# Kernel tuning notes

Measured on AMD Instinct MI355X. Metric: run time of the kernel, lower is better.

## Reference

```python
import jax, jax.numpy as jnp
import numpy as np

# dims: batch, seq(tokens, excl cls), input_dim, embed_dim, heads, ffn, experts, proto experts, classes
B, S, DIN, D, H, FF, E, P, NC = 2, 2048, 1024, 512, 8, 2048, 6, 4, 2
CAP = int(1.0 * S / E)  # capacity_factor=1.0


def _ln(x, g, b, eps=1e-5):
    m = x.mean(-1, keepdims=True)
    v = ((x - m) ** 2).mean(-1, keepdims=True)
    return (x - m) / jnp.sqrt(v + eps) * g + b


def _gelu(x):
    return jax.nn.gelu(x, approximate=False)


def _mha(x, in_w, in_b, out_w, out_b):
    # torch nn.MultiheadAttention, batch_first, eval (no dropout)
    b, s, d = x.shape
    dh = d // H
    qkv = x @ in_w.T + in_b
    q, k, v = jnp.split(qkv, 3, axis=-1)
    q = q.reshape(b, s, H, dh)
    k = k.reshape(b, s, H, dh)
    v = v.reshape(b, s, H, dh)
    att = jnp.einsum('bqhd,bkhd->bhqk', q, k) * (1.0 / np.sqrt(dh))
    att = jax.nn.softmax(att, axis=-1)
    o = jnp.einsum('bhqk,bkhd->bqhd', att, v).reshape(b, s, d)
    return o @ out_w.T + out_b


def _subln_ffn(x, w1, b1, lg, lb, w2, b2):
    # FeedForwardNetwork with subln: fc1 -> gelu -> LayerNorm -> fc2 (eval: no dropout)
    h = _gelu(x @ w1 + b1)
    h = _ln(h, lg, lb)
    return h @ w2 + b2


def _pamoe(x, gate_w, W1, b1, W2, b2):
    # top-1 prototype-augmented MoE with capacity-based token drop
    gate = jax.nn.softmax(x @ gate_w, axis=-1)          # [B,S,E]
    idx = jnp.argmax(gate, axis=-1)                      # [B,S]
    top_p = jnp.max(gate, axis=-1)                       # [B,S]
    oh = jax.nn.one_hot(idx, E, dtype=x.dtype)           # [B,S,E]
    pos = jnp.cumsum(oh, axis=1) * oh                    # position within expert
    keep = oh * (pos <= CAP)                             # capacity mask
    out = jnp.zeros_like(x)
    for e in range(E):  # small fixed loop over experts
        m = (keep[..., e] * top_p)[..., None]
        out = out + m * (_gelu(x @ W1[e] + b1[e]) @ W2[e] + b2[e])
    return out, gate


def _pamoe_ce(gate, labels):
    # CE between renormalized prototype-expert gate probs and cosine-sim labels
    p = gate[..., :P]
    logp = jnp.log(p / p.sum(-1, keepdims=True) + 1e-9)
    nll = -jnp.take_along_axis(logp, labels[..., None], axis=-1)[..., 0]
    return nll.mean()


def setup_inputs() -> dict:
    key = jax.random.key(0)
    cnt = [0]
    def nk():
        cnt[0] += 1
        return jax.random.fold_in(key, cnt[0])
    def w(*shape):
        return jax.random.normal(nk(), shape, dtype=jnp.float32) * 0.02
    d = {}
    d['x'] = jax.random.normal(nk(), (B, S, DIN), dtype=jnp.float32)
    d['protos'] = jax.random.normal(nk(), (P, DIN), dtype=jnp.float32)
    d['cls_token'] = jax.random.normal(nk(), (1, 1, D), dtype=jnp.float32)
    d['fc1_w'] = w(DIN, D); d['fc1_b'] = jnp.zeros((D,), jnp.float32)
    for li in ('l0', 'l1'):
        d[li + '_attn_in_w'] = w(3 * D, D); d[li + '_attn_in_b'] = jnp.zeros((3 * D,), jnp.float32)
        d[li + '_attn_out_w'] = w(D, D); d[li + '_attn_out_b'] = jnp.zeros((D,), jnp.float32)
        d[li + '_n1_g'] = jnp.ones((D,), jnp.float32); d[li + '_n1_b'] = jnp.zeros((D,), jnp.float32)
        d[li + '_n2_g'] = jnp.ones((D,), jnp.float32); d[li + '_n2_b'] = jnp.zeros((D,), jnp.float32)
    # layer0: pamoe + cls_ffn
    d['l0_cls_w1'] = w(D, FF); d['l0_cls_b1'] = jnp.zeros((FF,), jnp.float32)
    d['l0_cls_ln_g'] = jnp.ones((FF,), jnp.float32); d['l0_cls_ln_b'] = jnp.zeros((FF,), jnp.float32)
    d['l0_cls_w2'] = w(FF, D); d['l0_cls_b2'] = jnp.zeros((D,), jnp.float32)
    d['l0_gate_w'] = w(D, E)
    d['l0_e_w1'] = w(E, D, FF); d['l0_e_b1'] = jnp.zeros((E, FF), jnp.float32)
    d['l0_e_w2'] = w(E, FF, D); d['l0_e_b2'] = jnp.zeros((E, D), jnp.float32)
    # layer1: dense ffn
    d['l1_ffn_w1'] = w(D, FF); d['l1_ffn_b1'] = jnp.zeros((FF,), jnp.float32)
    d['l1_ffn_ln_g'] = jnp.ones((FF,), jnp.float32); d['l1_ffn_ln_b'] = jnp.zeros((FF,), jnp.float32)
    d['l1_ffn_w2'] = w(FF, D); d['l1_ffn_b2'] = jnp.zeros((D,), jnp.float32)
    d['norm_g'] = jnp.ones((D,), jnp.float32); d['norm_b'] = jnp.zeros((D,), jnp.float32)
    d['fc2_w'] = w(D, NC); d['fc2_b'] = jnp.zeros((NC,), jnp.float32)
    return d


def reference(x, protos, cls_token, fc1_w, fc1_b,
              l0_attn_in_w, l0_attn_in_b, l0_attn_out_w, l0_attn_out_b,
              l0_n1_g, l0_n1_b, l0_n2_g, l0_n2_b,
              l0_cls_w1, l0_cls_b1, l0_cls_ln_g, l0_cls_ln_b, l0_cls_w2, l0_cls_b2,
              l0_gate_w, l0_e_w1, l0_e_b1, l0_e_w2, l0_e_b2,
              l1_attn_in_w, l1_attn_in_b, l1_attn_out_w, l1_attn_out_b,
              l1_n1_g, l1_n1_b, l1_n2_g, l1_n2_b,
              l1_ffn_w1, l1_ffn_b1, l1_ffn_ln_g, l1_ffn_ln_b, l1_ffn_w2, l1_ffn_b2,
              norm_g, norm_b, fc2_w, fc2_b):
    # prototype cosine similarity on raw (detached) features -> routing supervision labels
    xr = jax.lax.stop_gradient(x)
    xn = xr / (jnp.linalg.norm(xr, axis=-1, keepdims=True) + 1e-8)
    pn = protos / (jnp.linalg.norm(protos, axis=-1, keepdims=True) + 1e-8)
    sim = jnp.einsum('bsd,pd->bsp', xn, pn)             # [B,S,P]
    labels = jnp.argmax(sim, axis=-1)                    # [B,S]

    h = x @ fc1_w + fc1_b                                # [B,S,D]
    cls = jnp.broadcast_to(cls_token, (h.shape[0], 1, D))
    h = jnp.concatenate([cls, h], axis=1)                # [B,S+1,D]

    # ---- layer 0 (pamoe block) ----
    attn = _mha(h, l0_attn_in_w, l0_attn_in_b, l0_attn_out_w, l0_attn_out_b)
    h = _ln(h, l0_n1_g, l0_n1_b)
    h = h + attn
    h = _ln(h, l0_n2_g, l0_n2_b)
    h_res = h
    c = _subln_ffn(h[:, 0:1], l0_cls_w1, l0_cls_b1, l0_cls_ln_g, l0_cls_ln_b, l0_cls_w2, l0_cls_b2)
    t, gate = _pamoe(h[:, 1:], l0_gate_w, l0_e_w1, l0_e_b1, l0_e_w2, l0_e_b2)
    h = h_res + jnp.concatenate([c, t], axis=1)          # pamoe residual
    loss_pamoe = _pamoe_ce(gate, labels)

    # ---- layer 1 (dense ffn block) ----
    attn = _mha(h, l1_attn_in_w, l1_attn_in_b, l1_attn_out_w, l1_attn_out_b)
    h = _ln(h, l1_n1_g, l1_n1_b)
    h = h + attn
    h = _ln(h, l1_n2_g, l1_n2_b)
    h = h + _subln_ffn(h, l1_ffn_w1, l1_ffn_b1, l1_ffn_ln_g, l1_ffn_ln_b, l1_ffn_w2, l1_ffn_b2)

    pooled = _ln(h, norm_g, norm_b)[:, 0]                # cls token
    logits = pooled @ fc2_w + fc2_b                      # [B,NC]
    return gate, logits, loss_pamoe
```

## Files before the change

### kernel.cpp

```cpp
#include <hip/hip_runtime.h>
#include <cmath>

#define DEVINL __device__ __forceinline__

typedef unsigned short ushort_t;
typedef unsigned int uint_t;

constexpr int Bb   = 2;
constexpr int Ss   = 2048;
constexpr int S1   = 2049;
constexpr int DIN  = 1024;
constexpr int Dd   = 512;
constexpr int Hh   = 8;
constexpr int FF   = 2048;
constexpr int Ee   = 6;
constexpr int NCc  = 2;
constexpr int CAP  = 341;
constexpr int NTOK = Bb * Ss;
constexpr int RR   = Bb * S1;
constexpr int MOE_ROWS = Bb * CAP;

typedef __attribute__((ext_vector_type(4))) float f32x4;
typedef __attribute__((ext_vector_type(8))) short bf16x8;

DEVINL float geluf(float x) { return 0.5f * x * (1.0f + erff(x * 0.7071067811865476f)); }

DEVINL ushort_t f2bf(float f) {
  uint_t u = __float_as_uint(f);
  u += 0x7FFFu + ((u >> 16) & 1u);
  return (ushort_t)(u >> 16);
}
DEVINL float bf2f(ushort_t u) { return __uint_as_float((uint_t)u << 16); }

DEVINL void glds16(const ushort_t* g, void* lds) {
  __builtin_amdgcn_global_load_lds(
      (const __attribute__((address_space(1))) void*)g,
      (__attribute__((address_space(3))) void*)lds, 16, 0, 0);
}

DEVINL float wsum(float v) {
#pragma unroll
  for (int off = 32; off; off >>= 1) v += __shfl_xor(v, off);
  return v;
}
DEVINL float bsum(float v, float* red) {
  v = wsum(v);
  int w = threadIdx.x >> 6;
  if ((threadIdx.x & 63) == 0) red[w] = v;
  __syncthreads();
  float r = red[0] + red[1] + red[2] + red[3];
  __syncthreads();
  return r;
}

__global__ __launch_bounds__(256) void cast_kernel(const float* __restrict__ in,
                                                   ushort_t* __restrict__ out, int n8) {
  int i = blockIdx.x * 256 + threadIdx.x;
  if (i >= n8) return;
  float4 a = *(const float4*)(in + (size_t)i * 8);
  float4 b = *(const float4*)(in + (size_t)i * 8 + 4);
  bf16x8 v;
  v[0] = (short)f2bf(a.x); v[1] = (short)f2bf(a.y);
  v[2] = (short)f2bf(a.z); v[3] = (short)f2bf(a.w);
  v[4] = (short)f2bf(b.x); v[5] = (short)f2bf(b.y);
  v[6] = (short)f2bf(b.z); v[7] = (short)f2bf(b.w);
  *(bf16x8*)(out + (size_t)i * 8) = v;
}

__global__ __launch_bounds__(256) void tpose_cast_kernel(const float* __restrict__ in,
                                                         ushort_t* __restrict__ outp,
                                                         int K, int N) {
  __shared__ float t[64][65];
  const int z = blockIdx.z;
  const float* src = in + (size_t)z * K * N;
  ushort_t* dst = outp + (size_t)z * K * N;
  const int k0 = blockIdx.x * 64, n0 = blockIdx.y * 64;
  const int tx = threadIdx.x & 15, ty = threadIdx.x >> 4;
#pragma unroll
  for (int p = 0; p < 4; ++p) {
    int k = ty + p * 16;
    float4 v = *(const float4*)(src + (size_t)(k0 + k) * N + n0 + tx * 4);
    t[k][tx * 4 + 0] = v.x; t[k][tx * 4 + 1] = v.y;
    t[k][tx * 4 + 2] = v.z; t[k][tx * 4 + 3] = v.w;
  }
  __syncthreads();
#pragma unroll
  for (int p = 0; p < 4; ++p) {
    int n = ty + p * 16;
    uint_t lo = (uint_t)f2bf(t[tx * 4 + 0][n]) | ((uint_t)f2bf(t[tx * 4 + 1][n]) << 16);
    uint_t hi = (uint_t)f2bf(t[tx * 4 + 2][n]) | ((uint_t)f2bf(t[tx * 4 + 3][n]) << 16);
    *(uint2*)(dst + (size_t)(n0 + n) * K + k0 + tx * 4) = make_uint2(lo, hi);
  }
}

__global__ __launch_bounds__(256) void labels_kernel(const float* __restrict__ x,
                                                     const float* __restrict__ protos,
                                                     int* __restrict__ lbl) {
  int t = blockIdx.x * 4 + (threadIdx.x >> 6);
  int lane = threadIdx.x & 63;
  if (t >= NTOK) return;
  const float* xr = x + (size_t)t * DIN;
  float xv[16];
  float ss = 0.f;
#pragma unroll
  for (int i = 0; i < 16; ++i) { xv[i] = xr[lane + 64 * i]; ss += xv[i] * xv[i]; }
  ss = wsum(ss);
  float nx = sqrtf(ss) + 1e-8f;
  float best = -2e30f; int bi = 0;
  for (int p = 0; p < 4; ++p) {
    const float* pr = protos + (size_t)p * DIN;
    float dp = 0.f, pp = 0.f;
#pragma unroll
    for (int i = 0; i < 16; ++i) { float v = pr[lane + 64 * i]; dp += v * xv[i]; pp += v * v; }
    dp = wsum(dp); pp = wsum(pp);
    float sim = dp / (nx * (sqrtf(pp) + 1e-8f));
    if (sim > best) { best = sim; bi = p; }
  }
  if (lane == 0) lbl[t] = bi;
}

template <bool ACT, bool SHIFT, int BMT>
__global__ __launch_bounds__(256) void mgemm_kernel(const ushort_t* __restrict__ A, int lda,
                                                    const ushort_t* __restrict__ Bw, int ldb,
                                                    const float* __restrict__ bias,
                                                    const ushort_t* __restrict__ res,
                                                    ushort_t* __restrict__ C, int ldc,
                                                    int M, int N, int K) {
  constexpr int MI = BMT / 32;
  __shared__ ushort_t As[BMT * 64];
  __shared__ ushort_t Bs[128 * 64];
  const int tid = threadIdx.x;
  const int l = tid & 63, l15 = l & 15, lg = l >> 4;
  const int w = tid >> 6;
  const int wm = w >> 1, wn = w & 1;
  const int bm = blockIdx.x * BMT, bn = blockIdx.y * 128;
  const int srowA = w * (BMT / 4) + (l >> 3);
  const int srowB = w * 32 + (l >> 3);
  const int scc = ((l & 7) ^ (l >> 3)) * 8;

  f32x4 acc[MI][4];
#pragma unroll
  for (int i = 0; i < MI; ++i)
#pragma unroll
    for (int j = 0; j < 4; ++j) acc[i][j] = (f32x4){0.f, 0.f, 0.f, 0.f};

  const ushort_t* agp[MI];
  const ushort_t* bgp[4];
#pragma unroll
  for (int j = 0; j < MI; ++j) {
    int ar = bm + srowA + j * 8; if (ar > M - 1) ar = M - 1;
    agp[j] = A + (size_t)ar * lda + scc;
  }
#pragma unroll
  for (int j = 0; j < 4; ++j)
    bgp[j] = Bw + (size_t)(bn + srowB + j * 8) * ldb + scc;

  for (int k0 = 0; k0 < K; k0 += 64) {
#pragma unroll
    for (int j = 0; j < MI; ++j)
      glds16(agp[j] + k0, (char*)As + w * (BMT * 32) + j * 1024);
#pragma unroll
    for (int j = 0; j < 4; ++j)
      glds16(bgp[j] + k0, (char*)Bs + w * 4096 + j * 1024);
    __syncthreads();
#pragma unroll
    for (int kc = 0; kc < 2; ++kc) {
      bf16x8 af[MI], bfr[4];
#pragma unroll
      for (int mi = 0; mi < MI; ++mi) {
        int row = wm * (BMT / 2) + mi * 16 + l15;
        af[mi] = *(const bf16x8*)((const char*)As +
                   ((row * 128 + (kc * 32 + lg * 8) * 2) ^ ((row & 7) << 4)));
      }
#pragma unroll
      for (int ni = 0; ni < 4; ++ni) {
        int row = wn * 64 + ni * 16 + l15;
        bfr[ni] = *(const bf16x8*)((const char*)Bs +
                   ((row * 128 + (kc * 32 + lg * 8) * 2) ^ ((row & 7) << 4)));
      }
#pragma unroll
      for (int mi = 0; mi < MI; ++mi)
#pragma unroll
        for (int ni = 0; ni < 4; ++ni)
          acc[mi][ni] = __builtin_amdgcn_mfma_f32_16x16x32_bf16(af[mi], bfr[ni], acc[mi][ni], 0, 0, 0);
    }
    __syncthreads();
  }

#pragma unroll
  for (int mi = 0; mi < MI; ++mi)
#pragma unroll
    for (int r = 0; r < 4; ++r) {
      int row = bm + wm * (BMT / 2) + mi * 16 + lg * 4 + r;
      if (row < M) {
        int orow = SHIFT ? (row + (row >> 11) + 1) : row;
#pragma unroll
        for (int ni = 0; ni < 4; ++ni) {
          int col = bn + wn * 64 + ni * 16 + l15;
          float t = acc[mi][ni][r];
          if (bias) t += bias[col];
          if (ACT) t = geluf(t);
          if (res) t += bf2f(res[(size_t)orow * ldc + col]);
          C[(size_t)orow * ldc + col] = f2bf(t);
        }
      }
    }
}

__global__ __launch_bounds__(256) void moe_mgemm1_kernel(const ushort_t* __restrict__ h2,
                                                         const ushort_t* __restrict__ w1T,
                                                         const float* __restrict__ b1all,
                                                         const int* __restrict__ list,
                                                         const int* __restrict__ cnt,
                                                         ushort_t* __restrict__ hid) {
  __shared__ ushort_t As[128 * 64];
  __shared__ ushort_t Bs[128 * 64];
  const int e = blockIdx.z;
  const int c0 = cnt[e * 2 + 0], c1 = cnt[e * 2 + 1];
  const ushort_t* Bw = w1T + (size_t)e * Dd * FF;
  const int tid = threadIdx.x;
  const int l = tid & 63, l15 = l & 15, lg = l >> 4;
  const int w = tid >> 6;
  const int wm = w >> 1, wn = w & 1;
  const int bm = blockIdx.x * 128, bn = blockIdx.y * 128;
  const int srow = w * 32 + (l >> 3);
  const int scc = ((l & 7) ^ (l >> 3)) * 8;

  f32x4 acc[4][4];
#pragma unroll
  for (int i = 0; i < 4; ++i)
#pragma unroll
    for (int j = 0; j < 4; ++j) acc[i][j] = (f32x4){0.f, 0.f, 0.f, 0.f};

  const ushort_t* agp[4];
  const ushort_t* bgp[4];
#pragma unroll
  for (int j = 0; j < 4; ++j) {
    int r = bm + srow + j * 8; if (r > MOE_ROWS - 1) r = MOE_ROWS - 1;
    int tok = list[e * MOE_ROWS + r] & (NTOK - 1);
    int b = tok >> 11, s = tok & (Ss - 1);
    agp[j] = h2 + (size_t)(b * S1 + s + 1) * Dd + scc;
    bgp[j] = Bw + (size_t)(bn + srow + j * 8) * Dd + scc;
  }

  for (int k0 = 0; k0 < Dd; k0 += 64) {
#pragma unroll
    for (int j = 0; j < 4; ++j) {
      glds16(agp[j] + k0, (char*)As + w * 4096 + j * 1024);
      glds16(bgp[j] + k0, (char*)Bs + w * 4096 + j * 1024);
    }
    __syncthreads();
#pragma unroll
    for (int kc = 0; kc < 2; ++kc) {
      bf16x8 af[4], bfr[4];
#pragma unroll
      for (int mi = 0; mi < 4; ++mi) {
        int row = wm * 64 + mi * 16 + l15;
        af[mi] = *(const bf16x8*)((const char*)As +
                   ((row * 128 + (kc * 32 + lg * 8) * 2) ^ ((row & 7) << 4)));
      }
#pragma unroll
      for (int ni = 0; ni < 4; ++ni) {
        int row = wn * 64 + ni * 16 + l15;
        bfr[ni] = *(const bf16x8*)((const char*)Bs +
                   ((row * 128 + (kc * 32 + lg * 8) * 2) ^ ((row & 7) << 4)));
      }
#pragma unroll
      for (int mi = 0; mi < 4; ++mi)
#pragma unroll
        for (int ni = 0; ni < 4; ++ni)
          acc[mi][ni] = __builtin_amdgcn_mfma_f32_16x16x32_bf16(af[mi], bfr[ni], acc[mi][ni], 0, 0, 0);
    }
    __syncthreads();
  }

#pragma unroll
  for (int mi = 0; mi < 4; ++mi)
#pragma unroll
    for (int rr = 0; rr < 4; ++rr) {
      int row = bm + wm * 64 + mi * 16 + lg * 4 + rr;
      bool v2 = (row < MOE_ROWS) && ((row < CAP) ? (row < c0) : ((row - CAP) < c1));
      if (v2) {
#pragma unroll
        for (int ni = 0; ni < 4; ++ni) {
          int col = bn + wn * 64 + ni * 16 + l15;
          hid[((size_t)e * MOE_ROWS + row) * FF + col] =
              f2bf(geluf(acc[mi][ni][rr] + b1all[e * FF + col]));
        }
      }
    }
}

template <int BMT>
__global__ __launch_bounds__(256) void moe_mgemm2_kernel(const ushort_t* __restrict__ hid,
                                                         const ushort_t* __restrict__ w2T,
                                                         const float* __restrict__ b2all,
                                                         const int* __restrict__ list,
                                                         const int* __restrict__ cnt,
                                                         const float* __restrict__ topp,
                                                         ushort_t* __restrict__ out) {
  constexpr int MI = BMT / 32;
  __shared__ ushort_t As[BMT * 64];
  __shared__ ushort_t Bs[128 * 64];
  const int e = blockIdx.z;
  const int c0 = cnt[e * 2 + 0], c1 = cnt[e * 2 + 1];
  const ushort_t* Bw = w2T + (size_t)e * FF * Dd;
  const int tid = threadIdx.x;
  const int l = tid & 63, l15 = l & 15, lg = l >> 4;
  const int w = tid >> 6;
  const int wm = w >> 1, wn = w & 1;
  const int bm = blockIdx.x * BMT, bn = blockIdx.y * 128;
  const int srowA = w * (BMT / 4) + (l >> 3);
  const int srowB = w * 32 + (l >> 3);
  const int scc = ((l & 7) ^ (l >> 3)) * 8;

  f32x4 acc[MI][4];
#pragma unroll
  for (int i = 0; i < MI; ++i)
#pragma unroll
    for (int j = 0; j < 4; ++j) acc[i][j] = (f32x4){0.f, 0.f, 0.f, 0.f};

  const ushort_t* agp[MI];
  const ushort_t* bgp[4];
#pragma unroll
  for (int j = 0; j < MI; ++j) {
    int r = bm + srowA + j * 8; if (r > MOE_ROWS - 1) r = MOE_ROWS - 1;
    agp[j] = hid + ((size_t)e * MOE_ROWS + r) * FF + scc;
  }
#pragma unroll
  for (int j = 0; j < 4; ++j)
    bgp[j] = Bw + (size_t)(bn + srowB + j * 8) * FF + scc;

  for (int k0 = 0; k0 < FF; k0 += 64) {
#pragma unroll
    for (int j = 0; j < MI; ++j)
      glds16(agp[j] + k0, (char*)As + w * (BMT * 32) + j * 1024);
#pragma unroll
    for (int j = 0; j < 4; ++j)
      glds16(bgp[j] + k0, (char*)Bs + w * 4096 + j * 1024);
    __syncthreads();
#pragma unroll
    for (int kc = 0; kc < 2; ++kc) {
      bf16x8 af[MI], bfr[4];
#pragma unroll
      for (int mi = 0; mi < MI; ++mi) {
        int row = wm * (BMT / 2) + mi * 16 + l15;
        af[mi] = *(const bf16x8*)((const char*)As +
                   ((row * 128 + (kc * 32 + lg * 8) * 2) ^ ((row & 7) << 4)));
      }
#pragma unroll
      for (int ni = 0; ni < 4; ++ni) {
        int row = wn * 64 + ni * 16 + l15;
        bfr[ni] = *(const bf16x8*)((const char*)Bs +
                   ((row * 128 + (kc * 32 + lg * 8) * 2) ^ ((row & 7) << 4)));
      }
#pragma unroll
      for (int mi = 0; mi < MI; ++mi)
#pragma unroll
        for (int ni = 0; ni < 4; ++ni)
          acc[mi][ni] = __builtin_amdgcn_mfma_f32_16x16x32_bf16(af[mi], bfr[ni], acc[mi][ni], 0, 0, 0);
    }
    __syncthreads();
  }

#pragma unroll
  for (int mi = 0; mi < MI; ++mi)
#pragma unroll
    for (int rr = 0; rr < 4; ++rr) {
      int row = bm + wm * (BMT / 2) + mi * 16 + lg * 4 + rr;
      bool v2 = (row < MOE_ROWS) && ((row < CAP) ? (row < c0) : ((row - CAP) < c1));
      if (v2) {
        int tok = list[e * MOE_ROWS + row];
        int b = tok >> 11, s = tok & (Ss - 1);
        float tp = topp[tok];
#pragma unroll
        for (int ni = 0; ni < 4; ++ni) {
          int col = bn + wn * 64 + ni * 16 + l15;
          size_t oidx = (size_t)(b * S1 + s + 1) * Dd + col;
          out[oidx] = f2bf(bf2f(out[oidx]) + tp * (acc[mi][ni][rr] + b2all[e * Dd + col]));
        }
      }
    }
}

__global__ __launch_bounds__(256) void cls_fill_kernel(const float* __restrict__ cls,
                                                       ushort_t* __restrict__ h) {
  int i = threadIdx.x;
  uint_t pk = (uint_t)f2bf(cls[i * 2]) | ((uint_t)f2bf(cls[i * 2 + 1]) << 16);
  *(uint_t*)(h + i * 2) = pk;
  *(uint_t*)(h + (size_t)S1 * Dd + i * 2) = pk;
}

template <int EPL>
__global__ __launch_bounds__(256) void ln_wave_kernel(const ushort_t* __restrict__ in,
                                                      const ushort_t* __restrict__ addv,
                                                      const float* __restrict__ g,
                                                      const float* __restrict__ bvec,
                                                      ushort_t* __restrict__ out,
                                                      ushort_t* __restrict__ out2,
                                                      int nrows) {
  constexpr int N = 64 * EPL;
  const int row = blockIdx.x * 4 + (threadIdx.x >> 6);
  const int lane = threadIdx.x & 63;
  if (row >= nrows) return;
  const size_t base = (size_t)row * N + lane * EPL;
  float xf[EPL];
  float s1 = 0.f, s2 = 0.f;
#pragma unroll
  for (int c = 0; c < EPL / 8; ++c) {
    bf16x8 x8 = *(const bf16x8*)(in + base + c * 8);
#pragma unroll
    for (int j = 0; j < 8; ++j) {
      float v = bf2f((ushort_t)x8[j]);
      xf[c * 8 + j] = v;
      s1 += v; s2 += v * v;
    }
  }
  s1 = wsum(s1); s2 = wsum(s2);
  float mean = s1 * (1.0f / N);
  float var = s2 * (1.0f / N) - mean * mean;
  float rstd = rsqrtf(var + 1e-5f);
#pragma unroll
  for (int c = 0; c < EPL / 8; ++c) {
    bf16x8 a8;
    if (addv) a8 = *(const bf16x8*)(addv + base + c * 8);
    bf16x8 o8;
#pragma unroll
    for (int j = 0; j < 8; ++j) {
      int col = lane * EPL + c * 8 + j;
      float v = (xf[c * 8 + j] - mean) * rstd * g[col] + bvec[col];
      if (addv) v += bf2f((ushort_t)a8[j]);
      o8[j] = (short)f2bf(v);
    }
    *(bf16x8*)(out + base + c * 8) = o8;
    if (out2) *(bf16x8*)(out2 + base + c * 8) = o8;
  }
}

__global__ __launch_bounds__(256) void ln2_wave_kernel(const ushort_t* __restrict__ in,
                                                       const ushort_t* __restrict__ addv,
                                                       const float* __restrict__ g1,
                                                       const float* __restrict__ b1,
                                                       const float* __restrict__ g2,
                                                       const float* __restrict__ b2,
                                                       ushort_t* __restrict__ out,
                                                       ushort_t* __restrict__ out2,
                                                       int nrows) {
  constexpr int N = 512;
  const int row = blockIdx.x * 4 + (threadIdx.x >> 6);
  const int lane = threadIdx.x & 63;
  if (row >= nrows) return;
  const size_t base = (size_t)row * N + lane * 8;
  bf16x8 x8 = *(const bf16x8*)(in + base);
  bf16x8 a8 = *(const bf16x8*)(addv + base);
  float xf[8];
  float s1 = 0.f, s2 = 0.f;
#pragma unroll
  for (int j = 0; j < 8; ++j) {
    float v = bf2f((ushort_t)x8[j]);
    xf[j] = v; s1 += v; s2 += v * v;
  }
  s1 = wsum(s1); s2 = wsum(s2);
  float mean = s1 * (1.0f / N);
  float rstd = rsqrtf(s2 * (1.0f / N) - mean * mean + 1e-5f);
  float vf[8];
  float t1 = 0.f, t2 = 0.f;
#pragma unroll
  for (int j = 0; j < 8; ++j) {
    int col = lane * 8 + j;
    float v = (xf[j] - mean) * rstd * g1[col] + b1[col] + bf2f((ushort_t)a8[j]);
    vf[j] = v; t1 += v; t2 += v * v;
  }
  t1 = wsum(t1); t2 = wsum(t2);
  float mean2 = t1 * (1.0f / N);
  float rstd2 = rsqrtf(t2 * (1.0f / N) - mean2 * mean2 + 1e-5f);
  bf16x8 o8;
#pragma unroll
  for (int j = 0; j < 8; ++j) {
    int col = lane * 8 + j;
    o8[j] = (short)f2bf((vf[j] - mean2) * rstd2 * g2[col] + b2[col]);
  }
  *(bf16x8*)(out + base) = o8;
  if (out2) *(bf16x8*)(out2 + base) = o8;
}

__global__ __launch_bounds__(256) void attn_mfma_kernel(const ushort_t* __restrict__ qkv,
                                                        ushort_t* __restrict__ o) {
  __shared__ ushort_t Ksh[64 * 64];
  __shared__ ushort_t Vt[64 * 64];
  const int tid = threadIdx.x;
  const int w = tid >> 6, l = tid & 63;
  const int l15 = l & 15, lg = l >> 4;
  const int hh = blockIdx.y, b = blockIdx.z;
  const int qblk = blockIdx.x * 64;
  const size_t rbase = (size_t)b * S1 * 1536;
  const float CEXP = 0.125f * 1.4426950408889634f;

  bf16x8 aq[2];
  {
    int qr = qblk + w * 16 + l15;
    const ushort_t* qp = qkv + rbase + (size_t)qr * 1536 + hh * 64;
#pragma unroll
    for (int dc = 0; dc < 2; ++dc)
      aq[dc] = (qr < S1) ? *(const bf16x8*)(qp + dc * 32 + lg * 8)
                         : (bf16x8){0, 0, 0, 0, 0, 0, 0, 0};
  }

  f32x4 ovac[4];
#pragma unroll
  for (int dt = 0; dt < 4; ++dt) ovac[dt] = (f32x4){0.f, 0.f, 0.f, 0.f};
  float m_r = -1e30f, l_r = 0.f;

  const int sk_r = tid >> 3, sk_c = tid & 7;
  const int sv_k0 = (tid & 31) * 2, sv_d0 = (tid >> 5) * 8;

  for (int c = 0; c < 33; ++c) {
#pragma unroll
    for (int pass = 0; pass < 2; ++pass) {
      int r = sk_r + pass * 32;
      int key = c * 64 + r;
      bf16x8 v;
      if (key < S1)
        v = *(const bf16x8*)(qkv + rbase + (size_t)key * 1536 + 512 + hh * 64 + sk_c * 8);
      else
        v = (bf16x8){0, 0, 0, 0, 0, 0, 0, 0};
      *(bf16x8*)((char*)Ksh + (((r * 64 + sk_c * 8) * 2) ^ ((r & 7) << 4))) = v;
    }
    {
      int key0 = c * 64 + sv_k0;
      const ushort_t* vp = qkv + rbase + (size_t)key0 * 1536 + 1024 + hh * 64 + sv_d0;
      bf16x8 va, vb;
      if (key0 < S1) va = *(const bf16x8*)(vp);
      else va = (bf16x8){0, 0, 0, 0, 0, 0, 0, 0};
      if (key0 + 1 < S1) vb = *(const bf16x8*)(vp + 1536);
      else vb = (bf16x8){0, 0, 0, 0, 0, 0, 0, 0};
#pragma unroll
      for (int i = 0; i < 8; ++i) {
        uint_t pk = (uint_t)(ushort_t)va[i] | ((uint_t)(ushort_t)vb[i] << 16);
        int d = sv_d0 + i;
        *(uint_t*)((char*)Vt + (((d * 64 + sv_k0) * 2) ^ ((d & 7) << 4))) = pk;
      }
    }
    __syncthreads();

    f32x4 s[4];
    __builtin_amdgcn_s_setprio(1);
#pragma unroll
    for (int kt = 0; kt < 4; ++kt) {
      f32x4 acc = (f32x4){0.f, 0.f, 0.f, 0.f};
      const int krow = kt * 16 + l15;
      const int rswz = (krow & 7) << 4;
#pragma unroll
      for (int dc = 0; dc < 2; ++dc) {
        bf16x8 kb = *(const bf16x8*)((const char*)Ksh + (((krow * 64 + dc * 32 + lg * 8) * 2) ^ rswz));
        acc = __builtin_amdgcn_mfma_f32_16x16x32_bf16(kb, aq[dc], acc, 0, 0, 0);
      }
      s[kt] = acc;
    }
    __builtin_amdgcn_s_setprio(0);
    if (c == 32) {
#pragma unroll
      for (int kt = 0; kt < 4; ++kt)
#pragma unroll
        for (int r = 0; r < 4; ++r)
          if (2048 + kt * 16 + lg * 4 + r >= S1) s[kt][r] = -1e30f;
    }

    f32x4 m4 = (f32x4){fmaxf(s[0][0], s[1][0]), fmaxf(s[0][1], s[1][1]),
                       fmaxf(s[0][2], s[1][2]), fmaxf(s[0][3], s[1][3])};
#pragma unroll
    for (int r = 0; r < 4; ++r) m4[r] = fmaxf(m4[r], fmaxf(s[2][r], s[3][r]));
    float mx = fmaxf(fmaxf(m4[0], m4[1]), fmaxf(m4[2], m4[3]));
    mx = fmaxf(mx, __shfl_xor(mx, 16));
    mx = fmaxf(mx, __shfl_xor(mx, 32));
    if (!__all(mx <= m_r + 8.0f)) {
      float mn = fmaxf(m_r, mx);
      float fac = __builtin_amdgcn_exp2f((m_r - mn) * CEXP);
      m_r = mn;
      float facq[4];
#pragma unroll
      for (int r = 0; r < 4; ++r) facq[r] = __shfl(fac, lg * 4 + r);
#pragma unroll
      for (int dt = 0; dt < 4; ++dt)
#pragma unroll
        for (int r = 0; r < 4; ++r) ovac[dt][r] *= facq[r];
      l_r *= fac;
    }
    float mc = m_r * CEXP;
    float p[4][4];
    float rs = 0.f;
#pragma unroll
    for (int kt = 0; kt < 4; ++kt)
#pragma unroll
      for (int r = 0; r < 4; ++r) {
        float pv = __builtin_amdgcn_exp2f(s[kt][r] * CEXP - mc);
        p[kt][r] = pv;
        rs += pv;
      }
    rs += __shfl_xor(rs, 16);
    rs += __shfl_xor(rs, 32);
    l_r += rs;

    uint_t pk[4][2];
#pragma unroll
    for (int kt = 0; kt < 4; ++kt) {
      pk[kt][0] = (uint_t)f2bf(p[kt][0]) | ((uint_t)f2bf(p[kt][1]) << 16);
      pk[kt][1] = (uint_t)f2bf(p[kt][2]) | ((uint_t)f2bf(p[kt][3]) << 16);
    }

    bf16x8 pa[2];
#pragma unroll
    for (int kh = 0; kh < 2; ++kh) {
      union { uint_t u[4]; bf16x8 v; } cu;
#pragma unroll
      for (int wd = 0; wd < 4; ++wd) {
        int src = (((2 * lg + (wd >> 1)) & 3) << 4) + l15;
        uint_t c0 = (uint_t)__shfl((int)pk[kh * 2 + 0][wd & 1], src);
        uint_t c1 = (uint_t)__shfl((int)pk[kh * 2 + 1][wd & 1], src);
        cu.u[wd] = (lg & 2) ? c1 : c0;
      }
      pa[kh] = cu.v;
    }

    __builtin_amdgcn_s_setprio(1);
#pragma unroll
    for (int kh = 0; kh < 2; ++kh)
#pragma unroll
      for (int dt = 0; dt < 4; ++dt) {
        const int vrow = dt * 16 + l15;
        bf16x8 vb = *(const bf16x8*)((const char*)Vt +
                      (((vrow * 64 + kh * 32 + lg * 8) * 2) ^ ((vrow & 7) << 4)));
        ovac[dt] = __builtin_amdgcn_mfma_f32_16x16x32_bf16(pa[kh], vb, ovac[dt], 0, 0, 0);
      }
    __builtin_amdgcn_s_setprio(0);
    __syncthreads();
  }

  float invq[4];
#pragma unroll
  for (int r = 0; r < 4; ++r) invq[r] = 1.0f / __shfl(l_r, lg * 4 + r);
#pragma unroll
  for (int r = 0; r < 4; ++r) {
    int qq = qblk + w * 16 + lg * 4 + r;
    if (qq < S1) {
      ushort_t* orow = o + (size_t)(b * S1 + qq) * Dd + hh * 64;
#pragma unroll
      for (int dt = 0; dt < 4; ++dt) orow[dt * 16 + l15] = f2bf(ovac[dt][r] * invq[r]);
    }
  }
}

__global__ __launch_bounds__(256) void gate_kernel(const ushort_t* __restrict__ h2,
                                                   const float* __restrict__ gw,
                                                   float* __restrict__ gate_out,
                                                   float* __restrict__ topp,
                                                   int* __restrict__ idx) {
  int t = blockIdx.x * 4 + (threadIdx.x >> 6);
  int lane = threadIdx.x & 63;
  if (t >= NTOK) return;
  int b = t >> 11, s = t & (Ss - 1);
  const ushort_t* hr = h2 + (size_t)(b * S1 + s + 1) * Dd;
  bf16x8 h8 = *(const bf16x8*)(hr + lane * 8);
  float acc[6] = {};
#pragma unroll
  for (int j = 0; j < 8; ++j) {
    int d = lane * 8 + j;
    float xv = bf2f((ushort_t)h8[j]);
    const float* g = gw + (size_t)d * Ee;
#pragma unroll
    for (int e = 0; e < 6; ++e) acc[e] += xv * g[e];
  }
#pragma unroll
  for (int e = 0; e < 6; ++e) acc[e] = wsum(acc[e]);
  if (lane == 0) {
    float mx = acc[0];
#pragma unroll
    for (int e = 1; e < 6; ++e) mx = fmaxf(mx, acc[e]);
    float ex[6], sum = 0.f;
#pragma unroll
    for (int e = 0; e < 6; ++e) { ex[e] = __expf(acc[e] - mx); sum += ex[e]; }
    float invs = 1.0f / sum;
    int best = 0; float bp = ex[0];
#pragma unroll
    for (int e = 1; e < 6; ++e) { if (ex[e] > bp) { bp = ex[e]; best = e; } }
#pragma unroll
    for (int e = 0; e < 6; ++e) gate_out[(size_t)t * Ee + e] = ex[e] * invs;
    topp[t] = bp * invs;
    idx[t] = best;
  }
}

__global__ __launch_bounds__(256) void route_kernel(const int* __restrict__ idx,
                                                    int* __restrict__ list,
                                                    int* __restrict__ cnt) {
  __shared__ int cnts[256];
  __shared__ int tot;
  const int e = blockIdx.x, b = blockIdx.y;
  const int tid = threadIdx.x;
  const int s0 = tid * 8;
  int loc[8];
  int c = 0;
#pragma unroll
  for (int j = 0; j < 8; ++j) {
    int t = b * Ss + s0 + j;
    if (idx[t] == e) loc[c++] = t;
  }
  cnts[tid] = c;
  __syncthreads();
  if (tid == 0) {
    int run = 0;
    for (int i = 0; i < 256; ++i) { int v = cnts[i]; cnts[i] = run; run += v; }
    tot = run;
  }
  __syncthreads();
  int base = cnts[tid];
  for (int j = 0; j < c; ++j) {
    int pos = base + j;
    if (pos < CAP) list[e * MOE_ROWS + b * CAP + pos] = loc[j];
  }
  if (tid == 0) cnt[e * Bb + b] = (tot < CAP) ? tot : CAP;
}

__global__ __launch_bounds__(256) void cls_ffn1_kernel(const ushort_t* __restrict__ h2,
                                                       const float* __restrict__ w1,
                                                       const float* __restrict__ b1,
                                                       float* __restrict__ chid) {
  __shared__ float hrow[Dd];
  __shared__ float red[8][32];
  const int b = blockIdx.y, tid = threadIdx.x;
  const int cl = tid & 31, kp = tid >> 5;
  const int col = blockIdx.x * 32 + cl;
  const ushort_t* hr = h2 + (size_t)(b * S1) * Dd;
  hrow[tid] = bf2f(hr[tid]);
  hrow[tid + 256] = bf2f(hr[tid + 256]);
  __syncthreads();
  float acc = 0.f;
#pragma unroll 8
  for (int j = 0; j < 64; ++j) {
    int d = kp * 64 + j;
    acc += hrow[d] * w1[(size_t)d * FF + col];
  }
  red[kp][cl] = acc;
  __syncthreads();
  if (kp == 0) {
    float s = b1[col];
#pragma unroll
    for (int i = 0; i < 8; ++i) s += red[i][cl];
    chid[b * FF + col] = geluf(s);
  }
}

__global__ __launch_bounds__(256) void cls_ln_kernel(const float* __restrict__ chid,
                                                     const float* __restrict__ lg,
                                                     const float* __restrict__ lb,
                                                     float* __restrict__ chln) {
  __shared__ float red[8];
  const int b = blockIdx.x, tid = threadIdx.x;
  const float* hr = chid + b * FF;
  float hv[8];
  float s1 = 0.f, s2 = 0.f;
#pragma unroll
  for (int j = 0; j < 8; ++j) {
    hv[j] = hr[tid + j * 256];
    s1 += hv[j]; s2 += hv[j] * hv[j];
  }
  s1 = bsum(s1, red);
  s2 = bsum(s2, red);
  float mean = s1 * (1.0f / FF);
  float rstd = rsqrtf(s2 * (1.0f / FF) - mean * mean + 1e-5f);
#pragma unroll
  for (int j = 0; j < 8; ++j) {
    int k = tid + j * 256;
    chln[b * FF + k] = (hv[j] - mean) * rstd * lg[k] + lb[k];
  }
}

__global__ __launch_bounds__(256) void cls_ffn2_kernel(const float* __restrict__ chln,
                                                       const float* __restrict__ w2,
                                                       const float* __restrict__ b2,
                                                       ushort_t* __restrict__ outbuf) {
  __shared__ float red[8][32];
  const int b = blockIdx.y, tid = threadIdx.x;
  const int cl = tid & 31, kp = tid >> 5;
  const int col = blockIdx.x * 32 + cl;
  const float* hr = chln + b * FF;
  float acc = 0.f;
#pragma unroll 8
  for (int j = 0; j < 256; ++j) {
    int k = kp * 256 + j;
    acc += hr[k] * w2[(size_t)k * Dd + col];
  }
  red[kp][cl] = acc;
  __syncthreads();
  if (kp == 0) {
    float s = b2[col];
#pragma unroll
    for (int i = 0; i < 8; ++i) s += red[i][cl];
    size_t oidx = (size_t)(b * S1) * Dd + col;
    outbuf[oidx] = f2bf(bf2f(outbuf[oidx]) + s);
  }
}

__global__ __launch_bounds__(256) void loss_part_kernel(const float* __restrict__ gate,
                                                        const int* __restrict__ lbl,
                                                        float* __restrict__ part) {
  __shared__ float red[8];
  int t = blockIdx.x * 256 + threadIdx.x;
  float v = 0.f;
  if (t < NTOK) {
    const float* p = gate + (size_t)t * Ee;
    float sum = p[0] + p[1] + p[2] + p[3];
    float pl = p[lbl[t]];
    v = -logf(pl / sum + 1e-9f);
  }
  v = bsum(v, red);
  if (threadIdx.x == 0) part[blockIdx.x] = v;
}

__global__ void loss_final_kernel(const float* __restrict__ part, float* __restrict__ out) {
  if (threadIdx.x == 0) {
    float s = 0.f;
    for (int i = 0; i < 16; ++i) s += part[i];
    out[NTOK * Ee + Bb * NCc] = s / (float)NTOK;
  }
}

__global__ __launch_bounds__(256) void final_head_kernel(const ushort_t* __restrict__ h,
                                                         const float* __restrict__ g,
                                                         const float* __restrict__ bvec,
                                                         const float* __restrict__ w,
                                                         const float* __restrict__ fb,
                                                         float* __restrict__ out) {
  __shared__ float red[8];
  int b = blockIdx.x, tid = threadIdx.x;
  const ushort_t* hr = h + (size_t)(b * S1) * Dd;
  float x0 = bf2f(hr[tid]), x1 = bf2f(hr[tid + 256]);
  float s1 = bsum(x0 + x1, red);
  float s2 = bsum(x0 * x0 + x1 * x1, red);
  float mean = s1 * (1.0f / Dd);
  float var = s2 * (1.0f / Dd) - mean * mean;
  float rstd = rsqrtf(var + 1e-5f);
  float p0 = (x0 - mean) * rstd * g[tid] + bvec[tid];
  float p1 = (x1 - mean) * rstd * g[tid + 256] + bvec[tid + 256];
  float l0 = p0 * w[tid * 2 + 0] + p1 * w[(tid + 256) * 2 + 0];
  float l1 = p0 * w[tid * 2 + 1] + p1 * w[(tid + 256) * 2 + 1];
  l0 = bsum(l0, red);
  l1 = bsum(l1, red);
  if (tid == 0) {
    out[NTOK * Ee + b * NCc + 0] = l0 + fb[0];
    out[NTOK * Ee + b * NCc + 1] = l1 + fb[1];
  }
}

extern "C" void kernel_launch(void* const* d_in, const int* in_sizes, int n_in,
                              void* d_out, int out_size, void* d_ws, size_t ws_size,
                              hipStream_t stream) {
  (void)in_sizes; (void)n_in; (void)out_size; (void)ws_size;
  const float* x       = (const float*)d_in[0];
  const float* protos  = (const float*)d_in[1];
  const float* cls_tok = (const float*)d_in[2];
  const float* fc1_w   = (const float*)d_in[3];
  const float* fc1_b   = (const float*)d_in[4];
  const float* a0_in_w = (const float*)d_in[5];
  const float* a0_in_b = (const float*)d_in[6];
  const float* a0_out_w= (const float*)d_in[7];
  const float* a0_out_b= (const float*)d_in[8];
  const float* n1g0    = (const float*)d_in[9];
  const float* n1b0    = (const float*)d_in[10];
  const float* n2g0    = (const float*)d_in[11];
  const float* n2b0    = (const float*)d_in[12];
  const float* a1_in_w = (const float*)d_in[13];
  const float* a1_in_b = (const float*)d_in[14];
  const float* a1_out_w= (const float*)d_in[15];
  const float* a1_out_b= (const float*)d_in[16];
  const float* n1g1    = (const float*)d_in[17];
  const float* n1b1    = (const float*)d_in[18];
  const float* n2g1    = (const float*)d_in[19];
  const float* n2b1    = (const float*)d_in[20];
  const float* cw1     = (const float*)d_in[21];
  const float* cb1     = (const float*)d_in[22];
  const float* clg     = (const float*)d_in[23];
  const float* clb     = (const float*)d_in[24];
  const float* cw2     = (const float*)d_in[25];
  const float* cb2     = (const float*)d_in[26];
  const float* gate_w  = (const float*)d_in[27];
  const float* ew1     = (const float*)d_in[28];
  const float* eb1     = (const float*)d_in[29];
  const float* ew2     = (const float*)d_in[30];
  const float* eb2     = (const float*)d_in[31];
  const float* fw1     = (const float*)d_in[32];
  const float* fb1     = (const float*)d_in[33];
  const float* flg     = (const float*)d_in[34];
  const float* flb     = (const float*)d_in[35];
  const float* fw2     = (const float*)d_in[36];
  const float* fb2     = (const float*)d_in[37];
  const float* ng      = (const float*)d_in[38];
  const float* nb      = (const float*)d_in[39];
  const float* fc2_w   = (const float*)d_in[40];
  const float* fc2_b   = (const float*)d_in[41];
  float* out = (float*)d_out;

  char* base = (char*)d_ws;
  size_t o = 0;
  auto alloc = [&](size_t bytes) -> void* {
    void* p = base + o;
    o += (bytes + 255) & ~(size_t)255;
    return p;
  };
  ushort_t* UB0  = (ushort_t*)alloc((size_t)RR * Dd * 2);
  ushort_t* UB1  = (ushort_t*)alloc((size_t)RR * Dd * 2);
  ushort_t* UB2  = (ushort_t*)alloc((size_t)RR * Dd * 2);
  ushort_t* BIGU = (ushort_t*)alloc((size_t)RR * FF * 2);
  ushort_t* XB   = (ushort_t*)alloc((size_t)NTOK * DIN * 2);
  ushort_t* WQ0  = (ushort_t*)alloc((size_t)3 * Dd * Dd * 2);
  ushort_t* WO0  = (ushort_t*)alloc((size_t)Dd * Dd * 2);
  ushort_t* WQ1  = (ushort_t*)alloc((size_t)3 * Dd * Dd * 2);
  ushort_t* WO1  = (ushort_t*)alloc((size_t)Dd * Dd * 2);
  ushort_t* WF1T = (ushort_t*)alloc((size_t)Dd * DIN * 2);
  ushort_t* WE1T = (ushort_t*)alloc((size_t)Ee * FF * Dd * 2);
  ushort_t* WE2T = (ushort_t*)alloc((size_t)Ee * Dd * FF * 2);
  ushort_t* WFW1T= (ushort_t*)alloc((size_t)FF * Dd * 2);
  ushort_t* WFW2T= (ushort_t*)alloc((size_t)Dd * FF * 2);
  float* TOPP = (float*)alloc(NTOK * 4);
  float* PART = (float*)alloc(64 * 4);
  float* CHID = (float*)alloc(Bb * FF * 4);
  float* CHLN = (float*)alloc(Bb * FF * 4);
  int* LBL  = (int*)alloc(NTOK * 4);
  int* IDX  = (int*)alloc(NTOK * 4);
  int* LIST = (int*)alloc(Ee * MOE_ROWS * 4);
  int* CNT  = (int*)alloc(Ee * Bb * 4);

  const int ln_grid = (RR + 3) / 4;

  cast_kernel<<<(NTOK * DIN / 8 + 255) / 256, 256, 0, stream>>>(x, XB, NTOK * DIN / 8);
  cast_kernel<<<(3 * Dd * Dd / 8 + 255) / 256, 256, 0, stream>>>(a0_in_w, WQ0, 3 * Dd * Dd / 8);
  cast_kernel<<<(Dd * Dd / 8 + 255) / 256, 256, 0, stream>>>(a0_out_w, WO0, Dd * Dd / 8);
  cast_kernel<<<(3 * Dd * Dd / 8 + 255) / 256, 256, 0, stream>>>(a1_in_w, WQ1, 3 * Dd * Dd / 8);
  cast_kernel<<<(Dd * Dd / 8 + 255) / 256, 256, 0, stream>>>(a1_out_w, WO1, Dd * Dd / 8);
  tpose_cast_kernel<<<dim3(DIN / 64, Dd / 64, 1), 256, 0, stream>>>(fc1_w, WF1T, DIN, Dd);
  tpose_cast_kernel<<<dim3(Dd / 64, FF / 64, Ee), 256, 0, stream>>>(ew1, WE1T, Dd, FF);
  tpose_cast_kernel<<<dim3(FF / 64, Dd / 64, Ee), 256, 0, stream>>>(ew2, WE2T, FF, Dd);
  tpose_cast_kernel<<<dim3(Dd / 64, FF / 64, 1), 256, 0, stream>>>(fw1, WFW1T, Dd, FF);
  tpose_cast_kernel<<<dim3(FF / 64, Dd / 64, 1), 256, 0, stream>>>(fw2, WFW2T, FF, Dd);

  labels_kernel<<<NTOK / 4, 256, 0, stream>>>(x, protos, LBL);
  mgemm_kernel<false, true, 64><<<dim3(64, 4), 256, 0, stream>>>(
      XB, DIN, WF1T, DIN, fc1_b, nullptr, UB0, Dd, NTOK, Dd, DIN);
  cls_fill_kernel<<<1, 256, 0, stream>>>(cls_tok, UB0);

  mgemm_kernel<false, false, 64><<<dim3(65, 12), 256, 0, stream>>>(
      UB0, Dd, WQ0, Dd, a0_in_b, nullptr, BIGU, 3 * Dd, RR, 3 * Dd, Dd);
  attn_mfma_kernel<<<dim3(33, Hh, Bb), 256, 0, stream>>>(BIGU, UB1);
  mgemm_kernel<false, false, 64><<<dim3(65, 4), 256, 0, stream>>>(
      UB1, Dd, WO0, Dd, a0_out_b, nullptr, UB2, Dd, RR, Dd, Dd);
  ln2_wave_kernel<<<ln_grid, 256, 0, stream>>>(UB0, UB2, n1g0, n1b0, n2g0, n2b0, UB0, UB2, RR);

  cls_ffn1_kernel<<<dim3(FF / 32, Bb), 256, 0, stream>>>(UB0, cw1, cb1, CHID);
  cls_ln_kernel<<<Bb, 256, 0, stream>>>(CHID, clg, clb, CHLN);
  cls_ffn2_kernel<<<dim3(Dd / 32, Bb), 256, 0, stream>>>(CHLN, cw2, cb2, UB2);
  gate_kernel<<<NTOK / 4, 256, 0, stream>>>(UB0, gate_w, out, TOPP, IDX);
  route_kernel<<<dim3(Ee, Bb), 256, 0, stream>>>(IDX, LIST, CNT);
  moe_mgemm1_kernel<<<dim3(6, 16, Ee), 256, 0, stream>>>(UB0, WE1T, eb1, LIST, CNT, BIGU);
  moe_mgemm2_kernel<64><<<dim3(11, 4, Ee), 256, 0, stream>>>(BIGU, WE2T, eb2, LIST, CNT, TOPP, UB2);
  loss_part_kernel<<<16, 256, 0, stream>>>(out, LBL, PART);
  loss_final_kernel<<<1, 64, 0, stream>>>(PART, out);

  mgemm_kernel<false, false, 64><<<dim3(65, 12), 256, 0, stream>>>(
      UB2, Dd, WQ1, Dd, a1_in_b, nullptr, BIGU, 3 * Dd, RR, 3 * Dd, Dd);
  attn_mfma_kernel<<<dim3(33, Hh, Bb), 256, 0, stream>>>(BIGU, UB1);
  mgemm_kernel<false, false, 64><<<dim3(65, 4), 256, 0, stream>>>(
      UB1, Dd, WO1, Dd, a1_out_b, nullptr, UB0, Dd, RR, Dd, Dd);
  ln2_wave_kernel<<<ln_grid, 256, 0, stream>>>(UB2, UB0, n1g1, n1b1, n2g1, n2b1, UB2, nullptr, RR);

  mgemm_kernel<true, false, 128><<<dim3(33, 16), 256, 0, stream>>>(
      UB2, Dd, WFW1T, Dd, fb1, nullptr, BIGU, FF, RR, FF, Dd);
  ln_wave_kernel<32><<<ln_grid, 256, 0, stream>>>(BIGU, nullptr, flg, flb, BIGU, nullptr, RR);
  mgemm_kernel<false, false, 64><<<dim3(65, 4), 256, 0, stream>>>(
      BIGU, FF, WFW2T, FF, fb2, UB2, UB0, Dd, RR, Dd, FF);

  final_head_kernel<<<Bb, 256, 0, stream>>>(UB0, ng, nb, fc2_w, fc2_b, out);
}
```

Measured before the change: 498.5 us.

## Widen attention key tiles to 128, load K via direct-to-LDS, merge cast launches

The attention kernel now processes 128 keys per iteration instead of 64, halving the number of barrier-separated iterations and softmax rescale checks. K is loaded straight into LDS with glds16 using an XOR-swizzled column mapping, with out-of-range keys clamped rather than zero-filled and then masked. The five fp32-to-bf16 cast launches are merged into one kernel that picks source and destination by index range, cutting launch overhead. In exchange LDS use and register pressure (16 score values per lane) both double, which may lower occupancy.

```diff
diff --git a/kernel.cpp b/kernel.cpp
--- a/kernel.cpp
+++ b/kernel.cpp
@@ -53,18 +53,31 @@
   return r;
 }
 
-__global__ __launch_bounds__(256) void cast_kernel(const float* __restrict__ in,
-                                                   ushort_t* __restrict__ out, int n8) {
+constexpr int C5_N0 = NTOK * DIN / 8;
+constexpr int C5_N1 = 3 * Dd * Dd / 8;
+constexpr int C5_N2 = Dd * Dd / 8;
+constexpr int C5_T  = C5_N0 + 2 * C5_N1 + 2 * C5_N2;
+__global__ __launch_bounds__(256) void cast5_kernel(const float* __restrict__ s0, ushort_t* __restrict__ d0,
+                                                    const float* __restrict__ s1, ushort_t* __restrict__ d1,
+                                                    const float* __restrict__ s2, ushort_t* __restrict__ d2,
+                                                    const float* __restrict__ s3, ushort_t* __restrict__ d3,
+                                                    const float* __restrict__ s4, ushort_t* __restrict__ d4) {
   int i = blockIdx.x * 256 + threadIdx.x;
-  if (i >= n8) return;
-  float4 a = *(const float4*)(in + (size_t)i * 8);
-  float4 b = *(const float4*)(in + (size_t)i * 8 + 4);
+  if (i >= C5_T) return;
+  const float* src; ushort_t* dst; int off;
+  if (i < C5_N0) { src = s0; dst = d0; off = i; }
+  else if (i < C5_N0 + C5_N1) { src = s1; dst = d1; off = i - C5_N0; }
+  else if (i < C5_N0 + C5_N1 + C5_N2) { src = s2; dst = d2; off = i - C5_N0 - C5_N1; }
+  else if (i < C5_N0 + 2 * C5_N1 + C5_N2) { src = s3; dst = d3; off = i - C5_N0 - C5_N1 - C5_N2; }
+  else { src = s4; dst = d4; off = i - C5_N0 - 2 * C5_N1 - C5_N2; }
+  float4 a = *(const float4*)(src + (size_t)off * 8);
+  float4 b = *(const float4*)(src + (size_t)off * 8 + 4);
   bf16x8 v;
   v[0] = (short)f2bf(a.x); v[1] = (short)f2bf(a.y);
   v[2] = (short)f2bf(a.z); v[3] = (short)f2bf(a.w);
   v[4] = (short)f2bf(b.x); v[5] = (short)f2bf(b.y);
   v[6] = (short)f2bf(b.z); v[7] = (short)f2bf(b.w);
-  *(bf16x8*)(out + (size_t)i * 8) = v;
+  *(bf16x8*)(dst + (size_t)off * 8) = v;
 }
 
 __global__ __launch_bounds__(256) void tpose_cast_kernel(const float* __restrict__ in,
@@ -486,8 +499,8 @@
 
 __global__ __launch_bounds__(256) void attn_mfma_kernel(const ushort_t* __restrict__ qkv,
                                                         ushort_t* __restrict__ o) {
-  __shared__ ushort_t Ksh[64 * 64];
-  __shared__ ushort_t Vt[64 * 64];
+  __shared__ ushort_t Ksh[128 * 64];
+  __shared__ ushort_t Vt[64 * 128];
   const int tid = threadIdx.x;
   const int w = tid >> 6, l = tid & 63;
   const int l15 = l & 15, lg = l >> 4;
@@ -511,42 +524,44 @@
   for (int dt = 0; dt < 4; ++dt) ovac[dt] = (f32x4){0.f, 0.f, 0.f, 0.f};
   float m_r = -1e30f, l_r = 0.f;
 
-  const int sk_r = tid >> 3, sk_c = tid & 7;
-  const int sv_k0 = (tid & 31) * 2, sv_d0 = (tid >> 5) * 8;
-
-  for (int c = 0; c < 33; ++c) {
-#pragma unroll
-    for (int pass = 0; pass < 2; ++pass) {
-      int r = sk_r + pass * 32;
-      int key = c * 64 + r;
-      bf16x8 v;
-      if (key < S1)
-        v = *(const bf16x8*)(qkv + rbase + (size_t)key * 1536 + 512 + hh * 64 + sk_c * 8);
-      else
-        v = (bf16x8){0, 0, 0, 0, 0, 0, 0, 0};
-      *(bf16x8*)((char*)Ksh + (((r * 64 + sk_c * 8) * 2) ^ ((r & 7) << 4))) = v;
-    }
+  const int kcc = ((l & 7) ^ (l >> 3)) * 8;
+  const int krloc = w * 32 + (l >> 3);
+  const int sv_k0 = (tid & 63) * 2, sv_d0 = (tid >> 6) * 16;
+
+  for (int it = 0; it < 17; ++it) {
     {
-      int key0 = c * 64 + sv_k0;
-      const ushort_t* vp = qkv + rbase + (size_t)key0 * 1536 + 1024 + hh * 64 + sv_d0;
-      bf16x8 va, vb;
-      if (key0 < S1) va = *(const bf16x8*)(vp);
-      else va = (bf16x8){0, 0, 0, 0, 0, 0, 0, 0};
-      if (key0 + 1 < S1) vb = *(const bf16x8*)(vp + 1536);
-      else vb = (bf16x8){0, 0, 0, 0, 0, 0, 0, 0};
+      int rb = it * 128 + krloc;
+#pragma unroll
+      for (int pass = 0; pass < 4; ++pass) {
+        int key = rb + pass * 8;
+        if (key > S1 - 1) key = S1 - 1;
+        glds16(qkv + rbase + (size_t)key * 1536 + 512 + hh * 64 + kcc,
+               (char*)Ksh + w * 4096 + pass * 1024);
+      }
+    }
+    {
+      int key0 = it * 128 + sv_k0;
+      int k0c = (key0 > S1 - 1) ? S1 - 1 : key0;
+      int k1c = (key0 + 1 > S1 - 1) ? S1 - 1 : key0 + 1;
+      const ushort_t* vp0 = qkv + rbase + (size_t)k0c * 1536 + 1024 + hh * 64 + sv_d0;
+      const ushort_t* vp1 = qkv + rbase + (size_t)k1c * 1536 + 1024 + hh * 64 + sv_d0;
+      bf16x8 va0 = *(const bf16x8*)(vp0), va1 = *(const bf16x8*)(vp0 + 8);
+      bf16x8 vb0 = *(const bf16x8*)(vp1), vb1 = *(const bf16x8*)(vp1 + 8);
 #pragma unroll
       for (int i = 0; i < 8; ++i) {
-        uint_t pk = (uint_t)(ushort_t)va[i] | ((uint_t)(ushort_t)vb[i] << 16);
-        int d = sv_d0 + i;
-        *(uint_t*)((char*)Vt + (((d * 64 + sv_k0) * 2) ^ ((d & 7) << 4))) = pk;
+        int d0 = sv_d0 + i, d1 = sv_d0 + 8 + i;
+        uint_t p0 = (uint_t)(ushort_t)va0[i] | ((uint_t)(ushort_t)vb0[i] << 16);
+        uint_t p1 = (uint_t)(ushort_t)va1[i] | ((uint_t)(ushort_t)vb1[i] << 16);
+        *(uint_t*)((char*)Vt + ((d0 * 256 + sv_k0 * 2) ^ ((d0 & 7) << 4))) = p0;
+        *(uint_t*)((char*)Vt + ((d1 * 256 + sv_k0 * 2) ^ ((d1 & 7) << 4))) = p1;
       }
     }
     __syncthreads();
 
-    f32x4 s[4];
+    f32x4 s[8];
     __builtin_amdgcn_s_setprio(1);
 #pragma unroll
-    for (int kt = 0; kt < 4; ++kt) {
+    for (int kt = 0; kt < 8; ++kt) {
       f32x4 acc = (f32x4){0.f, 0.f, 0.f, 0.f};
       const int krow = kt * 16 + l15;
       const int rswz = (krow & 7) << 4;
@@ -558,18 +573,19 @@
       s[kt] = acc;
     }
     __builtin_amdgcn_s_setprio(0);
-    if (c == 32) {
-#pragma unroll
-      for (int kt = 0; kt < 4; ++kt)
+    if (it == 16) {
+#pragma unroll
+      for (int kt = 0; kt < 8; ++kt)
 #pragma unroll
         for (int r = 0; r < 4; ++r)
           if (2048 + kt * 16 + lg * 4 + r >= S1) s[kt][r] = -1e30f;
     }
 
-    f32x4 m4 = (f32x4){fmaxf(s[0][0], s[1][0]), fmaxf(s[0][1], s[1][1]),
-                       fmaxf(s[0][2], s[1][2]), fmaxf(s[0][3], s[1][3])};
-#pragma unroll
-    for (int r = 0; r < 4; ++r) m4[r] = fmaxf(m4[r], fmaxf(s[2][r], s[3][r]));
+    f32x4 m4 = s[0];
+#pragma unroll
+    for (int kt = 1; kt < 8; ++kt)
+#pragma unroll
+      for (int r = 0; r < 4; ++r) m4[r] = fmaxf(m4[r], s[kt][r]);
     float mx = fmaxf(fmaxf(m4[0], m4[1]), fmaxf(m4[2], m4[3]));
     mx = fmaxf(mx, __shfl_xor(mx, 16));
     mx = fmaxf(mx, __shfl_xor(mx, 32));
@@ -587,30 +603,29 @@
       l_r *= fac;
     }
     float mc = m_r * CEXP;
-    float p[4][4];
     float rs = 0.f;
 #pragma unroll
-    for (int kt = 0; kt < 4; ++kt)
+    for (int kt = 0; kt < 8; ++kt)
 #pragma unroll
       for (int r = 0; r < 4; ++r) {
         float pv = __builtin_amdgcn_exp2f(s[kt][r] * CEXP - mc);
-        p[kt][r] = pv;
+        s[kt][r] = pv;
         rs += pv;
       }
     rs += __shfl_xor(rs, 16);
     rs += __shfl_xor(rs, 32);
     l_r += rs;
 
-    uint_t pk[4][2];
-#pragma unroll
-    for (int kt = 0; kt < 4; ++kt) {
-      pk[kt][0] = (uint_t)f2bf(p[kt][0]) | ((uint_t)f2bf(p[kt][1]) << 16);
-      pk[kt][1] = (uint_t)f2bf(p[kt][2]) | ((uint_t)f2bf(p[kt][3]) << 16);
-    }
-
-    bf16x8 pa[2];
-#pragma unroll
-    for (int kh = 0; kh < 2; ++kh) {
+    uint_t pk[8][2];
+#pragma unroll
+    for (int kt = 0; kt < 8; ++kt) {
+      pk[kt][0] = (uint_t)f2bf(s[kt][0]) | ((uint_t)f2bf(s[kt][1]) << 16);
+      pk[kt][1] = (uint_t)f2bf(s[kt][2]) | ((uint_t)f2bf(s[kt][3]) << 16);
+    }
+
+    bf16x8 pa[4];
+#pragma unroll
+    for (int kh = 0; kh < 4; ++kh) {
       union { uint_t u[4]; bf16x8 v; } cu;
 #pragma unroll
       for (int wd = 0; wd < 4; ++wd) {
@@ -624,12 +639,12 @@
 
     __builtin_amdgcn_s_setprio(1);
 #pragma unroll
-    for (int kh = 0; kh < 2; ++kh)
+    for (int kh = 0; kh < 4; ++kh)
 #pragma unroll
       for (int dt = 0; dt < 4; ++dt) {
         const int vrow = dt * 16 + l15;
         bf16x8 vb = *(const bf16x8*)((const char*)Vt +
-                      (((vrow * 64 + kh * 32 + lg * 8) * 2) ^ ((vrow & 7) << 4)));
+                      (((vrow * 256 + (kh * 32 + lg * 8) * 2)) ^ ((vrow & 7) << 4)));
         ovac[dt] = __builtin_amdgcn_mfma_f32_16x16x32_bf16(pa[kh], vb, ovac[dt], 0, 0, 0);
       }
     __builtin_amdgcn_s_setprio(0);
@@ -932,11 +947,8 @@
 
   const int ln_grid = (RR + 3) / 4;
 
-  cast_kernel<<<(NTOK * DIN / 8 + 255) / 256, 256, 0, stream>>>(x, XB, NTOK * DIN / 8);
-  cast_kernel<<<(3 * Dd * Dd / 8 + 255) / 256, 256, 0, stream>>>(a0_in_w, WQ0, 3 * Dd * Dd / 8);
-  cast_kernel<<<(Dd * Dd / 8 + 255) / 256, 256, 0, stream>>>(a0_out_w, WO0, Dd * Dd / 8);
-  cast_kernel<<<(3 * Dd * Dd / 8 + 255) / 256, 256, 0, stream>>>(a1_in_w, WQ1, 3 * Dd * Dd / 8);
-  cast_kernel<<<(Dd * Dd / 8 + 255) / 256, 256, 0, stream>>>(a1_out_w, WO1, Dd * Dd / 8);
+  cast5_kernel<<<(C5_T + 255) / 256, 256, 0, stream>>>(
+      x, XB, a0_in_w, WQ0, a0_out_w, WO0, a1_in_w, WQ1, a1_out_w, WO1);
   tpose_cast_kernel<<<dim3(DIN / 64, Dd / 64, 1), 256, 0, stream>>>(fc1_w, WF1T, DIN, Dd);
   tpose_cast_kernel<<<dim3(Dd / 64, FF / 64, Ee), 256, 0, stream>>>(ew1, WE1T, Dd, FF);
   tpose_cast_kernel<<<dim3(FF / 64, Dd / 64, Ee), 256, 0, stream>>>(ew2, WE2T, FF, Dd);
```

Result: no change. 491.2 us (-1.5%).
